# Kernel tuning notes

Hardware: AMD Instinct MI355X
Metric: run time of the kernel (lower is better)

Reference implementation:

```python
import jax, jax.numpy as jnp
import numpy as np

D = 1024
H = 16
DH = D // H

def setup_inputs() -> dict:
    key = jax.random.key(0)
    ks = jax.random.split(key, 9)
    s = 0.02
    return {
        "x": jax.random.normal(ks[0], (2, 2048, D), dtype=jnp.float32),
        "Wq": jax.random.normal(ks[1], (D, D), dtype=jnp.float32) * s,
        "bq": jnp.zeros((D,), dtype=jnp.float32),
        "Wk": jax.random.normal(ks[2], (D, D), dtype=jnp.float32) * s,
        "bk": jnp.zeros((D,), dtype=jnp.float32),
        "Wv": jax.random.normal(ks[3], (D, D), dtype=jnp.float32) * s,
        "bv": jnp.zeros((D,), dtype=jnp.float32),
        "Wo": jax.random.normal(ks[4], (D, D), dtype=jnp.float32) * s,
        "bo": jnp.zeros((D,), dtype=jnp.float32),
    }

def reference(x, Wq, bq, Wk, bk, Wv, bv, Wo, bo):
    B, S, Dm = x.shape
    def proj(W, b):
        # [B,S,D] -> [B,H,S,DH]
        return (x @ W + b).reshape(B, S, H, DH).transpose(0, 2, 1, 3)
    q = proj(Wq, bq)
    k = proj(Wk, bk)
    v = proj(Wv, bv)
    scale = 1.0 / np.sqrt(DH).astype(np.float32)
    raw = jnp.einsum('bhsd,bhtd->bhst', q, k) * scale  # [B,H,S,S]
    w = jax.nn.softmax(raw, axis=-1)
    out = jnp.einsum('bhst,bhtd->bhsd', w, v)          # [B,H,S,DH]
    out = out.transpose(0, 2, 1, 3).reshape(B, S, Dm)
    return out @ Wo + bo
```

## Files before the change

kernel.cpp:

```cpp
#include <hip/hip_runtime.h>
#include <math.h>

constexpr int Dm  = 1024;
constexpr int NH  = 16;
constexpr int SQ  = 2048;
constexpr int NB  = 2;

typedef float f32x4 __attribute__((ext_vector_type(4)));
typedef float f32x16 __attribute__((ext_vector_type(16)));
typedef short bf16x8 __attribute__((ext_vector_type(8)));
typedef __attribute__((address_space(3))) unsigned int lds_u32;
typedef __attribute__((address_space(1))) const unsigned int glb_u32;

__device__ __forceinline__ void gload_lds16(const void* g, void* l) {
    __builtin_amdgcn_global_load_lds((glb_u32*)(uintptr_t)g, (lds_u32*)(uintptr_t)l, 16, 0, 0);
}

__device__ __forceinline__ unsigned short bf_round(float x) {
    unsigned u = __float_as_uint(x);
    unsigned r = u + 0x7fffu + ((u >> 16) & 1u);
    return (unsigned short)(r >> 16);
}

__device__ __forceinline__ float exp2_fast(float x) {
    float r;
    asm("v_exp_f32 %0, %1" : "=v"(r) : "v"(x));
    return r;
}

__device__ __forceinline__ unsigned cvt_pk(float lo, float hi_) {
    unsigned r;
    asm("v_cvt_pk_bf16_f32 %0, %1, %2" : "=v"(r) : "v"(lo), "v"(hi_));
    return r;
}

__device__ __forceinline__ void permlane_swap(unsigned& a, unsigned& b) {
    asm volatile("v_permlane32_swap_b32 %0, %1" : "+v"(a), "+v"(b));
}

__device__ __forceinline__ bf16x8 make_frag(unsigned a, unsigned b, unsigned c, unsigned d) {
    union { unsigned u[4]; bf16x8 v; } uu;
    uu.u[0] = a; uu.u[1] = b; uu.u[2] = c; uu.u[3] = d;
    return uu.v;
}

__global__ __launch_bounds__(256) void prologue(const float* __restrict__ x,
                                                const float* __restrict__ Wq,
                                                const float* __restrict__ Wk,
                                                const float* __restrict__ Wv,
                                                const float* __restrict__ Wo,
                                                unsigned short* __restrict__ xb,
                                                unsigned short* __restrict__ wt) {
    const int z = blockIdx.z;
    const int tid = threadIdx.x;
    if (z == 4) {
        size_t base = ((size_t)blockIdx.y * 16 + blockIdx.x) * 16384;
#pragma unroll
        for (int it = 0; it < 8; ++it) {
            size_t i = base + (size_t)it * 2048 + (size_t)tid * 8;
            float4 a = *(const float4*)&x[i];
            float4 b = *(const float4*)&x[i + 4];
            unsigned short o8[8] __attribute__((aligned(16)));
            o8[0] = bf_round(a.x); o8[1] = bf_round(a.y); o8[2] = bf_round(a.z); o8[3] = bf_round(a.w);
            o8[4] = bf_round(b.x); o8[5] = bf_round(b.y); o8[6] = bf_round(b.z); o8[7] = bf_round(b.w);
            *(uint4*)&xb[i] = *(const uint4*)o8;
        }
        return;
    }
    const float* W = (z == 0) ? Wq : (z == 1) ? Wk : (z == 2) ? Wv : Wo;
    unsigned short* dst = wt + (size_t)z * Dm * Dm;
    __shared__ float T[64][65];
    const int k0 = blockIdx.x * 64, n0 = blockIdx.y * 64;
#pragma unroll
    for (int i = 0; i < 4; ++i) {
        int s = tid + i * 256;
        int kk = s >> 4, c = (s & 15) * 4;
        *(float4*)&T[kk][c] = *(const float4*)&W[(size_t)(k0 + kk) * Dm + n0 + c];
    }
    __syncthreads();
#pragma unroll
    for (int i = 0; i < 2; ++i) {
        int s = tid + i * 256;
        int n = s >> 3, c8 = (s & 7) * 8;
        unsigned short o8[8] __attribute__((aligned(16)));
#pragma unroll
        for (int j = 0; j < 8; ++j) o8[j] = bf_round(T[c8 + j][n]);
        *(uint4*)&dst[(size_t)(n0 + n) * Dm + k0 + c8] = *(const uint4*)o8;
    }
}

__global__ __launch_bounds__(512) void gemm_qkv192(
    const unsigned short* __restrict__ xb,
    const unsigned short* __restrict__ wt,
    const float* __restrict__ bq, const float* __restrict__ bk,
    const float* __restrict__ bv,
    unsigned short* __restrict__ qbuf, unsigned short* __restrict__ kbuf,
    unsigned short* __restrict__ vtbuf)
{
    __shared__ unsigned short Alds[2][256 * 64];
    __shared__ unsigned short Blds[2][192 * 64];

    const int tid = threadIdx.x;
    const int lane = tid & 63, wid = tid >> 6;
    const int wm = wid >> 2, wn = wid & 3;
    const int l15 = lane & 15, lg = lane >> 4;

    const int bid = blockIdx.x;
    const int swz = (bid & 7) * 32 + (bid >> 3);
    const int bx = swz & 15, by = swz >> 4;
    const int m0 = by * 256, n0 = bx * 192;

    const int srow = wid * 8 + (lane >> 3);
    const int scol = ((lane & 7) ^ ((lane >> 3) & 7)) * 8;

    const unsigned short* Abase = xb + (size_t)m0 * Dm;
    const unsigned short* Bbase = wt + (size_t)n0 * Dm;

#define STAGE_TILE(t)                                                              \
    do {                                                                           \
        const unsigned short* As_ = Abase + (t) * 64;                              \
        const unsigned short* Bs_ = Bbase + (t) * 64;                              \
        unsigned short* Ad_ = Alds[(t) & 1];                                       \
        unsigned short* Bd_ = Blds[(t) & 1];                                       \
        _Pragma("unroll")                                                          \
        for (int i_ = 0; i_ < 4; ++i_)                                             \
            gload_lds16(&As_[(size_t)(i_ * 64 + srow) * Dm + scol],                \
                        &Ad_[i_ * 4096 + wid * 512]);                              \
        _Pragma("unroll")                                                          \
        for (int i_ = 0; i_ < 3; ++i_)                                             \
            gload_lds16(&Bs_[(size_t)(i_ * 64 + srow) * Dm + scol],                \
                        &Bd_[i_ * 4096 + wid * 512]);                              \
    } while (0)

    f32x4 acc[8][3];
#pragma unroll
    for (int mr = 0; mr < 8; ++mr)
#pragma unroll
        for (int nr = 0; nr < 3; ++nr) acc[mr][nr] = (f32x4){0.f, 0.f, 0.f, 0.f};

    STAGE_TILE(0);
    asm volatile("s_waitcnt vmcnt(0)" ::: "memory");
    __builtin_amdgcn_s_barrier();

    for (int t = 0; t < Dm / 64; ++t) {
        unsigned short* Ad = Alds[t & 1];
        unsigned short* Bd = Blds[t & 1];
        if (t + 1 < Dm / 64) STAGE_TILE(t + 1);

        bf16x8 a_[4][2], b01[2][2], b2[2];

#define RD_A(qm, fr, ks) \
    (*(const bf16x8*)&Ad[(wm * 128 + (qm) * 64 + (fr) * 16 + l15) * 64 + \
                         ((((ks) * 4 + lg) ^ (l15 & 7)) * 8)])
#define RD_B(fc, ks) \
    (*(const bf16x8*)&Bd[(wn * 48 + (fc) * 16 + l15) * 64 + \
                         ((((ks) * 4 + lg) ^ (l15 & 7)) * 8)])

#pragma unroll
        for (int fr = 0; fr < 4; ++fr) {
            a_[fr][0] = RD_A(0, fr, 0); a_[fr][1] = RD_A(0, fr, 1);
        }
#pragma unroll
        for (int fc = 0; fc < 2; ++fc) {
            b01[fc][0] = RD_B(fc, 0); b01[fc][1] = RD_B(fc, 1);
        }
        __builtin_amdgcn_s_barrier();
        __builtin_amdgcn_s_setprio(1);
#pragma unroll
        for (int fr = 0; fr < 4; ++fr)
#pragma unroll
            for (int fc = 0; fc < 2; ++fc)
#pragma unroll
                for (int ks = 0; ks < 2; ++ks)
                    acc[fr][fc] = __builtin_amdgcn_mfma_f32_16x16x32_bf16(
                        a_[fr][ks], b01[fc][ks], acc[fr][fc], 0, 0, 0);
        __builtin_amdgcn_s_setprio(0);
        __builtin_amdgcn_s_barrier();

        b2[0] = RD_B(2, 0); b2[1] = RD_B(2, 1);
        __builtin_amdgcn_s_barrier();
        __builtin_amdgcn_s_setprio(1);
#pragma unroll
        for (int fr = 0; fr < 4; ++fr)
#pragma unroll
            for (int ks = 0; ks < 2; ++ks)
                acc[fr][2] = __builtin_amdgcn_mfma_f32_16x16x32_bf16(
                    a_[fr][ks], b2[ks], acc[fr][2], 0, 0, 0);
        __builtin_amdgcn_s_setprio(0);
        __builtin_amdgcn_s_barrier();

#pragma unroll
        for (int fr = 0; fr < 4; ++fr) {
            a_[fr][0] = RD_A(1, fr, 0); a_[fr][1] = RD_A(1, fr, 1);
        }
        __builtin_amdgcn_s_barrier();
        __builtin_amdgcn_s_setprio(1);
#pragma unroll
        for (int fr = 0; fr < 4; ++fr)
#pragma unroll
            for (int ks = 0; ks < 2; ++ks)
                acc[4 + fr][2] = __builtin_amdgcn_mfma_f32_16x16x32_bf16(
                    a_[fr][ks], b2[ks], acc[4 + fr][2], 0, 0, 0);
        __builtin_amdgcn_s_setprio(0);
        __builtin_amdgcn_s_barrier();

#pragma unroll
        for (int fc = 0; fc < 2; ++fc) {
            b01[fc][0] = RD_B(fc, 0); b01[fc][1] = RD_B(fc, 1);
        }
        __builtin_amdgcn_s_barrier();
        __builtin_amdgcn_s_setprio(1);
#pragma unroll
        for (int fr = 0; fr < 4; ++fr)
#pragma unroll
            for (int fc = 0; fc < 2; ++fc)
#pragma unroll
                for (int ks = 0; ks < 2; ++ks)
                    acc[4 + fr][fc] = __builtin_amdgcn_mfma_f32_16x16x32_bf16(
                        a_[fr][ks], b01[fc][ks], acc[4 + fr][fc], 0, 0, 0);
        __builtin_amdgcn_s_setprio(0);
        __builtin_amdgcn_s_barrier();

        asm volatile("s_waitcnt vmcnt(0)" ::: "memory");
        __builtin_amdgcn_s_barrier();
#undef RD_A
#undef RD_B
    }

    const float qscale = 0.18033688011f;
#pragma unroll
    for (int mr = 0; mr < 8; ++mr) {
#pragma unroll
        for (int nr = 0; nr < 3; ++nr) {
            const int m = m0 + wm * 128 + mr * 16 + lg * 4;
            const int nglob = n0 + wn * 48 + nr * 16 + l15;
            const int zq = nglob >> 10;
            const int nz = nglob & 1023;
            const float* bias = (zq == 0) ? bq : (zq == 1) ? bk : bv;
            const float bb_ = bias[nz];
            if (zq == 0) {
#pragma unroll
                for (int rr = 0; rr < 4; ++rr)
                    qbuf[(size_t)(m + rr) * Dm + nz] =
                        bf_round((acc[mr][nr][rr] + bb_) * qscale);
            } else if (zq == 1) {
#pragma unroll
                for (int rr = 0; rr < 4; ++rr)
                    kbuf[(size_t)(m + rr) * Dm + nz] = bf_round(acc[mr][nr][rr] + bb_);
            } else {
                const int bbv = m >> 11, s = m & (SQ - 1);
                const int hh = nz >> 6, d = nz & 63;
                unsigned short p4[4] __attribute__((aligned(8)));
#pragma unroll
                for (int rr = 0; rr < 4; ++rr) p4[rr] = bf_round(acc[mr][nr][rr] + bb_);
                *(uint2*)&vtbuf[(((size_t)bbv * NH + hh) * 64 + d) * SQ + s] =
                    *(const uint2*)p4;
            }
        }
    }
#undef STAGE_TILE
}

__device__ __forceinline__ void gemm_main(const unsigned short* __restrict__ A,
                                          const unsigned short* __restrict__ Bt,
                                          unsigned short* As, unsigned short* Bs,
                                          int m0, int n0, f32x4 acc[4][4]) {
    const int tid = threadIdx.x;
    const int lane = tid & 63, wid = tid >> 6;
    const int l15 = lane & 15, lg = lane >> 4;
    const int wr = (wid >> 1) * 64, wc = (wid & 1) * 64;

    for (int k0 = 0; k0 < Dm; k0 += 64) {
#pragma unroll
        for (int i = 0; i < 4; ++i) {
            int row = i * 32 + (tid >> 3);
            int sc8 = (tid & 7) * 8;
            int lbase = i * 2048 + wid * 512;
            gload_lds16(&A[(size_t)(m0 + row) * Dm + k0 + sc8], &As[lbase]);
            gload_lds16(&Bt[(size_t)(n0 + row) * Dm + k0 + sc8], &Bs[lbase]);
        }
        __syncthreads();
#pragma unroll
        for (int ks = 0; ks < 2; ++ks) {
            bf16x8 af[4], bfr[4];
#pragma unroll
            for (int r = 0; r < 4; ++r)
                af[r] = *(const bf16x8*)&As[(wr + r * 16 + l15) * 64 + ks * 32 + lg * 8];
#pragma unroll
            for (int c = 0; c < 4; ++c)
                bfr[c] = *(const bf16x8*)&Bs[(wc + c * 16 + l15) * 64 + ks * 32 + lg * 8];
#pragma unroll
            for (int r = 0; r < 4; ++r)
#pragma unroll
                for (int c = 0; c < 4; ++c)
                    acc[r][c] = __builtin_amdgcn_mfma_f32_16x16x32_bf16(af[r], bfr[c],
                                                                        acc[r][c], 0, 0, 0);
        }
        __syncthreads();
    }
}

__global__ __launch_bounds__(256) void gemm_out(const unsigned short* __restrict__ A,
                                                const unsigned short* __restrict__ Bt,
                                                const float* __restrict__ bias,
                                                float* __restrict__ Cf) {
    __shared__ unsigned short As[128 * 64];
    __shared__ unsigned short Bs[128 * 64];
    const int m0 = blockIdx.y * 128, n0 = blockIdx.x * 128;

    f32x4 acc[4][4];
#pragma unroll
    for (int r = 0; r < 4; ++r)
#pragma unroll
        for (int c = 0; c < 4; ++c) acc[r][c] = (f32x4){0.f, 0.f, 0.f, 0.f};

    gemm_main(A, Bt, As, Bs, m0, n0, acc);

    const int tid = threadIdx.x, lane = tid & 63, wid = tid >> 6;
    const int l15 = lane & 15, lg = lane >> 4;
    const int wr = (wid >> 1) * 64, wc = (wid & 1) * 64;
#pragma unroll
    for (int r = 0; r < 4; ++r) {
#pragma unroll
        for (int c = 0; c < 4; ++c) {
            const int mBase = m0 + wr + r * 16 + lg * 4;
            const int n = n0 + wc + c * 16 + l15;
            const float bv_ = bias[n];
#pragma unroll
            for (int rr = 0; rr < 4; ++rr)
                Cf[(size_t)(mBase + rr) * Dm + n] = acc[r][c][rr] + bv_;
        }
    }
}

__global__ __launch_bounds__(256) void attn_bf16(const unsigned short* q,
                                                 const unsigned short* __restrict__ k,
                                                 const unsigned short* __restrict__ vt,
                                                 unsigned short* ao) {
    __shared__ unsigned short KVs[2][2][64 * 64];
    const int qt = blockIdx.x, h = blockIdx.y, b = blockIdx.z;
    const int tid = threadIdx.x, lane = tid & 63, wid = tid >> 6;
    const int l31 = lane & 31, hi = lane >> 5;

    const size_t qrow0 = (size_t)b * SQ + qt * 128;
    const unsigned short* qp = q + (qrow0 + wid * 32 + l31) * Dm + h * 64;
    bf16x8 qf[4];
#pragma unroll
    for (int ks = 0; ks < 4; ++ks)
        qf[ks] = *(const bf16x8*)&qp[ks * 16 + hi * 8];

    const unsigned short* kb = k + (size_t)b * SQ * Dm + h * 64;
    const unsigned short* vb = vt + ((size_t)b * NH + h) * 64 * SQ;

    const int row0 = tid >> 3;
    const int s8 = (tid & 7) * 8;
    const int sw8 = (((tid & 7) ^ (row0 & 7))) * 8;
    const int koff0 = row0 * 64 + sw8;
    const int koff1 = (row0 + 32) * 64 + sw8;

    {
        uint4 k0v = *(const uint4*)&kb[(size_t)row0 * Dm + s8];
        uint4 k1v = *(const uint4*)&kb[(size_t)(row0 + 32) * Dm + s8];
        uint4 v0v = *(const uint4*)&vb[(size_t)row0 * SQ + s8];
        uint4 v1v = *(const uint4*)&vb[(size_t)(row0 + 32) * SQ + s8];
        *(uint4*)&KVs[0][0][koff0] = k0v; *(uint4*)&KVs[0][0][koff1] = k1v;
        *(uint4*)&KVs[0][1][koff0] = v0v; *(uint4*)&KVs[0][1][koff1] = v1v;
    }
    __syncthreads();

    const bf16x8 ones = make_frag(0x3F803F80u, 0x3F803F80u, 0x3F803F80u, 0x3F803F80u);
    f32x16 c0, c1, c2;
#pragma unroll
    for (int i = 0; i < 16; ++i) { c0[i] = 0.f; c1[i] = 0.f; c2[i] = 0.f; }

    int cur = 0;
    for (int t0 = 0; t0 < SQ; t0 += 64) {
        const bool hasNext = (t0 + 64) < SQ;
        uint4 kr0, kr1, vr0, vr1;
        if (hasNext) {
            const unsigned short* kn = kb + (size_t)(t0 + 64) * Dm;
            const unsigned short* vn = vb + (t0 + 64);
            kr0 = *(const uint4*)&kn[(size_t)row0 * Dm + s8];
            kr1 = *(const uint4*)&kn[(size_t)(row0 + 32) * Dm + s8];
            vr0 = *(const uint4*)&vn[(size_t)row0 * SQ + s8];
            vr1 = *(const uint4*)&vn[(size_t)(row0 + 32) * SQ + s8];
        }
        const unsigned short* Kc = KVs[cur][0];
        const unsigned short* Vc = KVs[cur][1];

#pragma unroll
        for (int kblk = 0; kblk < 2; ++kblk) {
            f32x16 p;
#pragma unroll
            for (int i = 0; i < 16; ++i) p[i] = 0.f;
            __builtin_amdgcn_s_setprio(1);
#pragma unroll
            for (int ks = 0; ks < 4; ++ks) {
                int row = kblk * 32 + l31;
                int slot = ((ks * 2 + hi) ^ (l31 & 7)) * 8;
                bf16x8 kf = *(const bf16x8*)&Kc[row * 64 + slot];
                p = __builtin_amdgcn_mfma_f32_32x32x16_bf16(kf, qf[ks], p, 0, 0, 0);
            }
            __builtin_amdgcn_s_setprio(0);

            float e[16];
#pragma unroll
            for (int i = 0; i < 16; ++i) e[i] = exp2_fast(p[i]);
            unsigned w0 = cvt_pk(e[0], e[1]),   w1 = cvt_pk(e[2], e[3]);
            unsigned w2 = cvt_pk(e[4], e[5]),   w3 = cvt_pk(e[6], e[7]);
            unsigned w4 = cvt_pk(e[8], e[9]),   w5 = cvt_pk(e[10], e[11]);
            unsigned w6 = cvt_pk(e[12], e[13]), w7 = cvt_pk(e[14], e[15]);
            permlane_swap(w0, w2); permlane_swap(w1, w3);
            permlane_swap(w4, w6); permlane_swap(w5, w7);
            bf16x8 pf0 = make_frag(w0, w1, w2, w3);
            bf16x8 pf1 = make_frag(w4, w5, w6, w7);

            int s0 = ((kblk * 4 + hi) ^ (l31 & 7)) * 8;
            int s1 = ((kblk * 4 + 2 + hi) ^ (l31 & 7)) * 8;
            bf16x8 va0 = *(const bf16x8*)&Vc[l31 * 64 + s0];
            bf16x8 va1 = *(const bf16x8*)&Vc[l31 * 64 + s1];
            bf16x8 vb0 = *(const bf16x8*)&Vc[(32 + l31) * 64 + s0];
            bf16x8 vb1 = *(const bf16x8*)&Vc[(32 + l31) * 64 + s1];
            __builtin_amdgcn_s_setprio(1);
            c0 = __builtin_amdgcn_mfma_f32_32x32x16_bf16(va0, pf0, c0, 0, 0, 0);
            c1 = __builtin_amdgcn_mfma_f32_32x32x16_bf16(vb0, pf0, c1, 0, 0, 0);
            c2 = __builtin_amdgcn_mfma_f32_32x32x16_bf16(ones, pf0, c2, 0, 0, 0);
            c0 = __builtin_amdgcn_mfma_f32_32x32x16_bf16(va1, pf1, c0, 0, 0, 0);
            c1 = __builtin_amdgcn_mfma_f32_32x32x16_bf16(vb1, pf1, c1, 0, 0, 0);
            c2 = __builtin_amdgcn_mfma_f32_32x32x16_bf16(ones, pf1, c2, 0, 0, 0);
            __builtin_amdgcn_s_setprio(0);
        }

        if (hasNext) {
            unsigned short* Kn = KVs[cur ^ 1][0];
            unsigned short* Vn = KVs[cur ^ 1][1];
            *(uint4*)&Kn[koff0] = kr0; *(uint4*)&Kn[koff1] = kr1;
            *(uint4*)&Vn[koff0] = vr0; *(uint4*)&Vn[koff1] = vr1;
        }
        __syncthreads();
        cur ^= 1;
    }

    float inv = 1.f / c2[0];

    unsigned short* Olds = (unsigned short*)KVs;
    {
        const int orow = wid * 32 + l31;
#pragma unroll
        for (int db = 0; db < 2; ++db) {
#pragma unroll
            for (int i = 0; i < 8; ++i) {
                float lo  = (db ? c1[2 * i] : c0[2 * i]) * inv;
                float hi_ = (db ? c1[2 * i + 1] : c0[2 * i + 1]) * inv;
                unsigned w = cvt_pk(lo, hi_);
                int d7 = hi * 4 + (i & 1) * 2;
                int slot = db * 4 + (i >> 1);
                int sw = slot ^ (l31 & 7);
                *(unsigned*)&Olds[orow * 64 + sw * 8 + d7] = w;
            }
        }
    }
    __syncthreads();
    {
        int r = tid >> 1, half = tid & 1;
        unsigned short* dst = ao + (qrow0 + r) * Dm + h * 64 + half * 32;
#pragma unroll
        for (int j = 0; j < 4; ++j) {
            int slot = half * 4 + j;
            int sw = slot ^ (r & 7);
            *(uint4*)&dst[j * 8] = *(const uint4*)&Olds[r * 64 + sw * 8];
        }
    }
}

extern "C" void kernel_launch(void* const* d_in, const int* in_sizes, int n_in,
                              void* d_out, int out_size, void* d_ws, size_t ws_size,
                              hipStream_t stream) {
    const float* x  = (const float*)d_in[0];
    const float* Wq = (const float*)d_in[1];
    const float* bq = (const float*)d_in[2];
    const float* Wk = (const float*)d_in[3];
    const float* bk = (const float*)d_in[4];
    const float* Wv = (const float*)d_in[5];
    const float* bv = (const float*)d_in[6];
    const float* Wo = (const float*)d_in[7];
    const float* bo = (const float*)d_in[8];
    float* out = (float*)d_out;

    const size_t M = (size_t)NB * SQ;
    const size_t elems = M * Dm;
    unsigned short* xb    = (unsigned short*)d_ws;
    unsigned short* wtb   = xb + elems;
    unsigned short* qbuf  = wtb + 4ull * Dm * Dm;
    unsigned short* kbuf  = qbuf + elems;
    unsigned short* vtbuf = kbuf + elems;

    dim3 blk(256);
    hipLaunchKernelGGL(prologue, dim3(16, 16, 5), blk, 0, stream,
                       x, Wq, Wk, Wv, Wo, xb, wtb);

    hipLaunchKernelGGL(gemm_qkv192, dim3(256), dim3(512), 0, stream,
                       xb, wtb, bq, bk, bv, qbuf, kbuf, vtbuf);

    hipLaunchKernelGGL(attn_bf16, dim3(SQ / 128, NH, NB), blk, 0, stream,
                       qbuf, kbuf, vtbuf, qbuf);

    hipLaunchKernelGGL(gemm_out, dim3(Dm / 128, M / 128), blk, 0, stream,
                       qbuf, wtb + 3ull * Dm * Dm, bo, out);
}
```

Baseline: 123.3 us.

## Double-buffer output GEMM with swizzled LDS and compute softmax sum on VALU

The output projection GEMM now double-buffers its LDS tiles, prefetching the next K tile with direct-to-LDS loads while the current one is consumed. It also XOR-swizzles the LDS layout to reduce bank conflicts and splits the MFMA work into two phases around barriers with raised priority. Separately, the attention kernel stops spending two MFMAs per block on a ones-vector row sum and instead accumulates the softmax denominator in scalar registers, combining the two half-waves with a cross-lane shuffle. The trade is more barriers in the GEMM and extra VALU adds in attention, in exchange for fewer matrix instructions and better load/compute overlap.

```diff
diff --git a/kernel.cpp b/kernel.cpp
--- a/kernel.cpp
+++ b/kernel.cpp
@@ -261,64 +261,106 @@
 #undef STAGE_TILE
 }
 
-__device__ __forceinline__ void gemm_main(const unsigned short* __restrict__ A,
-                                          const unsigned short* __restrict__ Bt,
-                                          unsigned short* As, unsigned short* Bs,
-                                          int m0, int n0, f32x4 acc[4][4]) {
+__global__ __launch_bounds__(256) void gemm_out8(const unsigned short* __restrict__ A,
+                                                 const unsigned short* __restrict__ Bt,
+                                                 const float* __restrict__ bias,
+                                                 float* __restrict__ Cf) {
+    __shared__ unsigned short Alds[2][128 * 64];
+    __shared__ unsigned short Blds[2][128 * 64];
+
     const int tid = threadIdx.x;
     const int lane = tid & 63, wid = tid >> 6;
     const int l15 = lane & 15, lg = lane >> 4;
     const int wr = (wid >> 1) * 64, wc = (wid & 1) * 64;
-
-    for (int k0 = 0; k0 < Dm; k0 += 64) {
-#pragma unroll
-        for (int i = 0; i < 4; ++i) {
-            int row = i * 32 + (tid >> 3);
-            int sc8 = (tid & 7) * 8;
-            int lbase = i * 2048 + wid * 512;
-            gload_lds16(&A[(size_t)(m0 + row) * Dm + k0 + sc8], &As[lbase]);
-            gload_lds16(&Bt[(size_t)(n0 + row) * Dm + k0 + sc8], &Bs[lbase]);
-        }
-        __syncthreads();
-#pragma unroll
-        for (int ks = 0; ks < 2; ++ks) {
-            bf16x8 af[4], bfr[4];
-#pragma unroll
-            for (int r = 0; r < 4; ++r)
-                af[r] = *(const bf16x8*)&As[(wr + r * 16 + l15) * 64 + ks * 32 + lg * 8];
-#pragma unroll
-            for (int c = 0; c < 4; ++c)
-                bfr[c] = *(const bf16x8*)&Bs[(wc + c * 16 + l15) * 64 + ks * 32 + lg * 8];
-#pragma unroll
-            for (int r = 0; r < 4; ++r)
-#pragma unroll
-                for (int c = 0; c < 4; ++c)
-                    acc[r][c] = __builtin_amdgcn_mfma_f32_16x16x32_bf16(af[r], bfr[c],
-                                                                        acc[r][c], 0, 0, 0);
-        }
-        __syncthreads();
-    }
-}
-
-__global__ __launch_bounds__(256) void gemm_out(const unsigned short* __restrict__ A,
-                                                const unsigned short* __restrict__ Bt,
-                                                const float* __restrict__ bias,
-                                                float* __restrict__ Cf) {
-    __shared__ unsigned short As[128 * 64];
-    __shared__ unsigned short Bs[128 * 64];
     const int m0 = blockIdx.y * 128, n0 = blockIdx.x * 128;
 
+    const int srow = (tid >> 3) & 31;
+    const int scol = ((tid & 7) ^ (srow & 7)) * 8;
+
+    const unsigned short* Abase = A + (size_t)m0 * Dm;
+    const unsigned short* Bbase = Bt + (size_t)n0 * Dm;
+
+#define STAGE_TILE(t)                                                              \
+    do {                                                                           \
+        const unsigned short* As_ = Abase + (t) * 64;                              \
+        const unsigned short* Bs_ = Bbase + (t) * 64;                              \
+        unsigned short* Ad_ = Alds[(t) & 1];                                       \
+        unsigned short* Bd_ = Blds[(t) & 1];                                       \
+        _Pragma("unroll")                                                          \
+        for (int i_ = 0; i_ < 4; ++i_) {                                           \
+            gload_lds16(&As_[(size_t)(i_ * 32 + srow) * Dm + scol],                \
+                        &Ad_[i_ * 2048 + wid * 512]);                              \
+            gload_lds16(&Bs_[(size_t)(i_ * 32 + srow) * Dm + scol],                \
+                        &Bd_[i_ * 2048 + wid * 512]);                              \
+        }                                                                          \
+    } while (0)
+
     f32x4 acc[4][4];
 #pragma unroll
     for (int r = 0; r < 4; ++r)
 #pragma unroll
         for (int c = 0; c < 4; ++c) acc[r][c] = (f32x4){0.f, 0.f, 0.f, 0.f};
 
-    gemm_main(A, Bt, As, Bs, m0, n0, acc);
-
-    const int tid = threadIdx.x, lane = tid & 63, wid = tid >> 6;
-    const int l15 = lane & 15, lg = lane >> 4;
-    const int wr = (wid >> 1) * 64, wc = (wid & 1) * 64;
+    STAGE_TILE(0);
+    asm volatile("s_waitcnt vmcnt(0)" ::: "memory");
+    __builtin_amdgcn_s_barrier();
+
+    for (int t = 0; t < Dm / 64; ++t) {
+        unsigned short* Ad = Alds[t & 1];
+        unsigned short* Bd = Blds[t & 1];
+        if (t + 1 < Dm / 64) STAGE_TILE(t + 1);
+
+        bf16x8 a_[4][2], b_[2][2];
+
+#define RD_A(fr, ks) \
+    (*(const bf16x8*)&Ad[(wr + (fr) * 16 + l15) * 64 + ((((ks) * 4 + lg) ^ (l15 & 7)) * 8)])
+#define RD_B(fc, ks) \
+    (*(const bf16x8*)&Bd[(wc + (fc) * 16 + l15) * 64 + ((((ks) * 4 + lg) ^ (l15 & 7)) * 8)])
+
+#pragma unroll
+        for (int fr = 0; fr < 4; ++fr) {
+            a_[fr][0] = RD_A(fr, 0); a_[fr][1] = RD_A(fr, 1);
+        }
+#pragma unroll
+        for (int fc = 0; fc < 2; ++fc) {
+            b_[fc][0] = RD_B(fc, 0); b_[fc][1] = RD_B(fc, 1);
+        }
+        __builtin_amdgcn_s_barrier();
+        __builtin_amdgcn_s_setprio(1);
+#pragma unroll
+        for (int fr = 0; fr < 4; ++fr)
+#pragma unroll
+            for (int fc = 0; fc < 2; ++fc)
+#pragma unroll
+                for (int ks = 0; ks < 2; ++ks)
+                    acc[fr][fc] = __builtin_amdgcn_mfma_f32_16x16x32_bf16(
+                        a_[fr][ks], b_[fc][ks], acc[fr][fc], 0, 0, 0);
+        __builtin_amdgcn_s_setprio(0);
+        __builtin_amdgcn_s_barrier();
+
+#pragma unroll
+        for (int fc = 0; fc < 2; ++fc) {
+            b_[fc][0] = RD_B(2 + fc, 0); b_[fc][1] = RD_B(2 + fc, 1);
+        }
+        __builtin_amdgcn_s_barrier();
+        __builtin_amdgcn_s_setprio(1);
+#pragma unroll
+        for (int fr = 0; fr < 4; ++fr)
+#pragma unroll
+            for (int fc = 0; fc < 2; ++fc)
+#pragma unroll
+                for (int ks = 0; ks < 2; ++ks)
+                    acc[fr][2 + fc] = __builtin_amdgcn_mfma_f32_16x16x32_bf16(
+                        a_[fr][ks], b_[fc][ks], acc[fr][2 + fc], 0, 0, 0);
+        __builtin_amdgcn_s_setprio(0);
+        __builtin_amdgcn_s_barrier();
+
+        asm volatile("s_waitcnt vmcnt(0)" ::: "memory");
+        __builtin_amdgcn_s_barrier();
+#undef RD_A
+#undef RD_B
+    }
+
 #pragma unroll
     for (int r = 0; r < 4; ++r) {
 #pragma unroll
@@ -331,6 +373,7 @@
                 Cf[(size_t)(mBase + rr) * Dm + n] = acc[r][c][rr] + bv_;
         }
     }
+#undef STAGE_TILE
 }
 
 __global__ __launch_bounds__(256) void attn_bf16(const unsigned short* q,
@@ -368,10 +411,10 @@
     }
     __syncthreads();
 
-    const bf16x8 ones = make_frag(0x3F803F80u, 0x3F803F80u, 0x3F803F80u, 0x3F803F80u);
-    f32x16 c0, c1, c2;
-#pragma unroll
-    for (int i = 0; i < 16; ++i) { c0[i] = 0.f; c1[i] = 0.f; c2[i] = 0.f; }
+    float psum = 0.f;
+    f32x16 c0, c1;
+#pragma unroll
+    for (int i = 0; i < 16; ++i) { c0[i] = 0.f; c1[i] = 0.f; }
 
     int cur = 0;
     for (int t0 = 0; t0 < SQ; t0 += 64) {
@@ -405,7 +448,7 @@
 
             float e[16];
 #pragma unroll
-            for (int i = 0; i < 16; ++i) e[i] = exp2_fast(p[i]);
+            for (int i = 0; i < 16; ++i) { e[i] = exp2_fast(p[i]); psum += e[i]; }
             unsigned w0 = cvt_pk(e[0], e[1]),   w1 = cvt_pk(e[2], e[3]);
             unsigned w2 = cvt_pk(e[4], e[5]),   w3 = cvt_pk(e[6], e[7]);
             unsigned w4 = cvt_pk(e[8], e[9]),   w5 = cvt_pk(e[10], e[11]);
@@ -423,11 +466,9 @@
             bf16x8 vb1 = *(const bf16x8*)&Vc[(32 + l31) * 64 + s1];
             __builtin_amdgcn_s_setprio(1);
             c0 = __builtin_amdgcn_mfma_f32_32x32x16_bf16(va0, pf0, c0, 0, 0, 0);
+            c0 = __builtin_amdgcn_mfma_f32_32x32x16_bf16(va1, pf1, c0, 0, 0, 0);
             c1 = __builtin_amdgcn_mfma_f32_32x32x16_bf16(vb0, pf0, c1, 0, 0, 0);
-            c2 = __builtin_amdgcn_mfma_f32_32x32x16_bf16(ones, pf0, c2, 0, 0, 0);
-            c0 = __builtin_amdgcn_mfma_f32_32x32x16_bf16(va1, pf1, c0, 0, 0, 0);
             c1 = __builtin_amdgcn_mfma_f32_32x32x16_bf16(vb1, pf1, c1, 0, 0, 0);
-            c2 = __builtin_amdgcn_mfma_f32_32x32x16_bf16(ones, pf1, c2, 0, 0, 0);
             __builtin_amdgcn_s_setprio(0);
         }
 
@@ -441,7 +482,8 @@
         cur ^= 1;
     }
 
-    float inv = 1.f / c2[0];
+    float s = psum + __shfl_xor(psum, 32, 64);
+    float inv = 1.f / s;
 
     unsigned short* Olds = (unsigned short*)KVs;
     {
@@ -505,6 +547,6 @@
     hipLaunchKernelGGL(attn_bf16, dim3(SQ / 128, NH, NB), blk, 0, stream,
                        qbuf, kbuf, vtbuf, qbuf);
 
-    hipLaunchKernelGGL(gemm_out, dim3(Dm / 128, M / 128), blk, 0, stream,
+    hipLaunchKernelGGL(gemm_out8, dim3(Dm / 128, M / 128), blk, 0, stream,
                        qbuf, wtb + 3ull * Dm * Dm, bo, out);
 }
```

Measured after the change: 116.6 us. -5.5%, faster.
